# Kernel tuning notes

Hardware: AMD Instinct MI355X
Metric: run time of the kernel (lower is better)

## Reference

```python
import jax, jax.numpy as jnp
import numpy as np

L = 32      # num_layer
N_ORD = 64  # order_of_a_LTImodel
U = 64      # u_size
Y = 64      # y_size
T = 8192    # sequence length
SCALE = 0.05  # keep block-bidiagonal A spectrally stable over 8192 steps


def setup_inputs() -> dict:
    key = jax.random.key(0)
    k_u, k_a, k_b0, k_bl, k_c = jax.random.split(key, 5)
    inp = {
        "input": jax.random.normal(k_u, (T, U), dtype=jnp.float32),
        # per-layer A_i weights (diagonal blocks)
        "A_stack": jax.random.normal(k_a, (L, N_ORD, N_ORD), dtype=jnp.float32) * SCALE,
        # layer-0 B (maps u -> state)
        "B0": jax.random.normal(k_b0, (N_ORD, U), dtype=jnp.float32) * SCALE,
        # layer i>=1 B weights (sub-diagonal coupling blocks)
        "B_lower": jax.random.normal(k_bl, (L - 1, N_ORD, N_ORD), dtype=jnp.float32) * SCALE,
        # per-layer C_i weights, concatenated along columns in forward
        "C_stack": jax.random.normal(k_c, (L, Y, N_ORD), dtype=jnp.float32),
        # D is frozen zeros (feedthrough=False)
        "D_w": jnp.zeros((Y, U), dtype=jnp.float32),
    }
    return inp


def _assemble(A_stack, B0, B_lower, C_stack):
    l, n, _ = A_stack.shape
    S = l * n
    A = jnp.zeros((S, S), A_stack.dtype)
    for i in range(l):  # fixed small structural loop
        A = A.at[i * n:(i + 1) * n, i * n:(i + 1) * n].set(A_stack[i])
    for i in range(1, l):
        A = A.at[i * n:(i + 1) * n, (i - 1) * n:i * n].set(B_lower[i - 1])
    B = jnp.concatenate([B0, jnp.zeros((S - n, B0.shape[1]), B0.dtype)], axis=0)
    # torch.cat([C_i], dim=1): [Y, L*n]
    C = jnp.transpose(C_stack, (1, 0, 2)).reshape(C_stack.shape[1], S)
    return A, B, C


def reference(input, A_stack, B0, B_lower, C_stack, D_w):
    A, B, C = _assemble(A_stack, B0, B_lower, C_stack)
    S = A.shape[0]
    x0 = jnp.zeros((S,), input.dtype)

    def step(x, u):
        y = C @ x + D_w @ u      # output BEFORE state update (y_t uses x_t)
        x_next = A @ x + B @ u
        return x_next, y

    _, ys = jax.lax.scan(step, x0, input)
    return ys  # [T, Y]
```

## Files before the change

### kernel.cpp

```cpp
#include <hip/hip_runtime.h>


#define LYR 32
#define NO  64
#define TSEQ 8192
#define JT  16
#define KD  (JT*NO)
#define PROWS (TSEQ+JT)
#define PBUF ((size_t)PROWS*NO)
#define FD  4

typedef _Float16 h16;
typedef _Float16 h16x8 __attribute__((ext_vector_type(8)));
typedef float    f32x4 __attribute__((ext_vector_type(4)));

__global__ __launch_bounds__(256) void prep1(
    const float* __restrict__ u, const float* __restrict__ B0,
    const float* __restrict__ Bl, const float* __restrict__ Cst,
    h16* __restrict__ pall, h16* __restrict__ ccast, float* __restrict__ kf32)
{
    int idx = blockIdx.x*256 + threadIdx.x;
    const int n_pad0 = JT*NO;
    const int n_u    = TSEQ*NO;
    const int n_c    = LYR*NO*NO;
    const int n_k    = LYR*NO*NO;
    const int n_zp   = 32*JT*NO;
    int total = n_pad0 + n_u + n_c + n_k + n_zp;
    for (; idx < total; idx += gridDim.x*256) {
        int e = idx;
        if (e < n_pad0) { pall[e] = (h16)0.f; continue; }
        e -= n_pad0;
        if (e < n_u) { pall[n_pad0 + e] = (h16)u[e]; continue; }
        e -= n_u;
        if (e < n_c) { ccast[e] = (h16)Cst[e]; continue; }
        e -= n_c;
        if (e < n_k) {
            int i = e >> 12;
            int r = e & 4095;
            kf32[((size_t)i*JT)*4096 + r] = (i == 0) ? B0[r] : Bl[e - 4096];
            continue;
        }
        e -= n_k;
        int b = e >> 10;
        int off = e & 1023;
        pall[(size_t)(b+1)*PBUF + off] = (h16)0.f;
    }
}

__global__ __launch_bounds__(256) void build_step(
    const float* __restrict__ A_stack, float* __restrict__ kf32,
    float* __restrict__ apow, int s)
{
    int h = 1 << s;
    int extra = (s < 3) ? 1 : 0;
    int slots = h + extra;
    int layer = blockIdx.x / slots;
    int q     = blockIdx.x % slots;
    const float* X = (s == 0) ? (A_stack + (size_t)layer*4096)
                              : (apow + ((size_t)layer*4 + (s-1))*4096);
    const float* Yop;
    float* Z;
    if (q < h) { Yop = kf32 + ((size_t)layer*JT + q)*4096;
                 Z   = kf32 + ((size_t)layer*JT + h + q)*4096; }
    else       { Yop = X;
                 Z   = apow + ((size_t)layer*4 + s)*4096; }

    __shared__ float lx[64*68];
    __shared__ float ly[64*68];
    int tid = threadIdx.x;
    for (int e = tid; e < 4096; e += 256) {
        int r = e >> 6, c = e & 63;
        lx[r*68 + c] = X[e];
        ly[r*68 + c] = Yop[e];
    }
    __syncthreads();
    int r0 = (tid >> 4) << 2;
    int c0 = (tid & 15) << 2;
    float acc[4][4] = {};
    for (int k = 0; k < 64; k++) {
        float a0 = lx[(r0+0)*68 + k];
        float a1 = lx[(r0+1)*68 + k];
        float a2 = lx[(r0+2)*68 + k];
        float a3 = lx[(r0+3)*68 + k];
        f32x4 bv = *(const f32x4*)&ly[k*68 + c0];
        #pragma unroll
        for (int j = 0; j < 4; j++) {
            acc[0][j] += a0*bv[j]; acc[1][j] += a1*bv[j];
            acc[2][j] += a2*bv[j]; acc[3][j] += a3*bv[j];
        }
    }
    #pragma unroll
    for (int i2 = 0; i2 < 4; i2++) {
        f32x4 o; o[0]=acc[i2][0]; o[1]=acc[i2][1]; o[2]=acc[i2][2]; o[3]=acc[i2][3];
        *(f32x4*)&Z[(size_t)(r0+i2)*64 + c0] = o;
    }
}

__global__ __launch_bounds__(256) void castK(const float* __restrict__ kf32,
                                             h16* __restrict__ kt)
{
    int idx = blockIdx.x*256 + threadIdx.x;
    const int total = LYR*NO*KD;
    for (; idx < total; idx += gridDim.x*256) {
        int i   = idx >> 16;
        int rem = idx & 65535;
        int n   = rem >> 10;
        int kap = rem & 1023;
        int jp  = kap >> 6, m = kap & 63;
        int j   = JT-1-jp;
        kt[idx] = (h16)kf32[(((size_t)i*JT + j)*64 + n)*64 + m];
    }
}

template<int S>
__device__ __forceinline__ void phase_body(
    const h16* inb, h16* outb, const h16* __restrict__ kb,
    h16* __restrict__ gout, const int w0, float* red, const int tid)
{
    const int wv = tid >> 6, lane = tid & 63, r = lane & 15, q = lane >> 4;
    const h16* abase = inb + (r + wv*4)*72 + q*8;
    const h16* bbase = kb + (size_t)r*KD + wv*256 + q*8;
#define LDA(s, ls) (*(const h16x8*)(abase + ((s)*16 + ((ls)>>1))*72 + ((ls)&1)*32))
#define LDB(c, ls) (*(const h16x8*)(bbase + (c)*(16*KD) + (ls)*32))
    f32x4 acc[S][4] = {};
    h16x8 a0[S], b0[4], a1[S], b1[4];
    #pragma unroll
    for (int s = 0; s < S; s++) { a0[s]=LDA(s,0); a1[s]=LDA(s,1); }
    #pragma unroll
    for (int c = 0; c < 4; c++) { b0[c]=LDB(c,0); b1[c]=LDB(c,1); }
    #pragma unroll 1
    for (int h2 = 0; h2 < 4; h2++) {
        int pE = 2*h2 + 2; pE = pE > 7 ? 7 : pE;
        int pO = 2*h2 + 3; pO = pO > 7 ? 7 : pO;
        h16x8 ca[S], cb[4];
        #pragma unroll
        for (int s = 0; s < S; s++) ca[s] = a0[s];
        #pragma unroll
        for (int c = 0; c < 4; c++) cb[c] = b0[c];
        #pragma unroll
        for (int s = 0; s < S; s++) a0[s] = LDA(s, pE);
        #pragma unroll
        for (int c = 0; c < 4; c++) b0[c] = LDB(c, pE);
        #pragma unroll
        for (int s = 0; s < S; s++)
            #pragma unroll
            for (int c = 0; c < 4; c++)
                acc[s][c] = __builtin_amdgcn_mfma_f32_16x16x32_f16(ca[s], cb[c], acc[s][c], 0,0,0);
        #pragma unroll
        for (int s = 0; s < S; s++) ca[s] = a1[s];
        #pragma unroll
        for (int c = 0; c < 4; c++) cb[c] = b1[c];
        #pragma unroll
        for (int s = 0; s < S; s++) a1[s] = LDA(s, pO);
        #pragma unroll
        for (int c = 0; c < 4; c++) b1[c] = LDB(c, pO);
        #pragma unroll
        for (int s = 0; s < S; s++)
            #pragma unroll
            for (int c = 0; c < 4; c++)
                acc[s][c] = __builtin_amdgcn_mfma_f32_16x16x32_f16(ca[s], cb[c], acc[s][c], 0,0,0);
    }
#undef LDA
#undef LDB
    const int cb2 = (tid & 7) << 3;
    #pragma unroll
    for (int ch = 0; ch < (S+1)/2; ch++) {
        const int sbase = ch*2;
        const int nt = (S - sbase) < 2 ? (S - sbase) : 2;
        __syncthreads();
        if (wv >= 2) {
            float* myred = red + (size_t)(wv-2)*(32*68);
            #pragma unroll
            for (int s2 = 0; s2 < 2; s2++) if (s2 < nt)
                #pragma unroll
                for (int c = 0; c < 4; c++)
                    #pragma unroll
                    for (int g = 0; g < 4; g++)
                        myred[(s2*16 + q*4 + g)*68 + c*16 + r] = acc[sbase+s2][c][g];
        }
        __syncthreads();
        if (wv < 2) {
            float* myred = red + (size_t)wv*(32*68);
            #pragma unroll
            for (int s2 = 0; s2 < 2; s2++) if (s2 < nt)
                #pragma unroll
                for (int c = 0; c < 4; c++)
                    #pragma unroll
                    for (int g = 0; g < 4; g++)
                        myred[(s2*16 + q*4 + g)*68 + c*16 + r] += acc[sbase+s2][c][g];
        }
        __syncthreads();
        for (int w = tid >> 3; w < nt*16; w += 32) {
            f32x4 u0 = *(const f32x4*)&red[w*68 + cb2];
            f32x4 u1 = *(const f32x4*)&red[w*68 + cb2 + 4];
            f32x4 v0 = *(const f32x4*)&red[32*68 + w*68 + cb2];
            f32x4 v1 = *(const f32x4*)&red[32*68 + w*68 + cb2 + 4];
            u0 += v0; u1 += v1;
            h16 ov[8];
            #pragma unroll
            for (int j = 0; j < 4; j++) { ov[j] = (h16)u0[j]; ov[4+j] = (h16)u1[j]; }
            const int W = sbase*16 + w;
            if (outb) *(int4*)&outb[W*72 + cb2] = *(int4*)&ov[0];
            const unsigned wrel = (unsigned)(W - w0);
            if (wrel < 32u) *(int4*)&gout[(size_t)wrel*64 + cb2] = *(int4*)&ov[0];
        }
    }
    __syncthreads();
}

__global__ __launch_bounds__(256) void stage4(
    h16* pall, const h16* __restrict__ kt, int i0)
{
    __shared__ __align__(16) h16   bufA[96*72];
    __shared__ __align__(16) h16   bufB[96*72];
    __shared__ __align__(16) float red[2*32*68];
    const int tid = threadIdx.x;
    const size_t t0 = (size_t)blockIdx.x * 32;

    const h16* pin = pall + (size_t)i0*PBUF;
    for (int e = tid; e < 96*8; e += 256) {
        int rr = e >> 3, cc = e & 7;
        long g = (long)t0 - 48 + rr;
        int4 v = make_int4(0,0,0,0);
        if (g >= 0) v = *(const int4*)&pin[(size_t)g*64 + cc*8];
        *(int4*)&bufA[rr*72 + cc*8] = v;
    }
    __syncthreads();

    h16* g1 = pall + (size_t)(i0+1)*PBUF + (JT + t0)*64;
    h16* g2 = pall + (size_t)(i0+2)*PBUF + (JT + t0)*64;
    h16* g3 = pall + (size_t)(i0+3)*PBUF + (JT + t0)*64;
    h16* g4 = pall + (size_t)(i0+4)*PBUF + (JT + t0)*64;
    const h16* k1 = kt + (size_t)(i0+0)*NO*KD;
    const h16* k2 = kt + (size_t)(i0+1)*NO*KD;
    const h16* k3 = kt + (size_t)(i0+2)*NO*KD;
    const h16* k4 = kt + (size_t)(i0+3)*NO*KD;

    phase_body<5>(bufA, bufB, k1, g1, 48, red, tid);
    phase_body<4>(bufB, bufA, k2, g2, 32, red, tid);
    phase_body<3>(bufA, bufB, k3, g3, 16, red, tid);
    phase_body<2>(bufB, (h16*)0, k4, g4, 0, red, tid);
}

__global__ __launch_bounds__(256, 2) void y_final(
    const h16* __restrict__ pall, const h16* __restrict__ ccast,
    float* __restrict__ out)
{
    __shared__ __align__(16) float red[2*32*68];
    int tid = threadIdx.x;
    size_t t0 = (size_t)blockIdx.x * 32;
    int wv = tid >> 6, lane = tid & 63, r = lane & 15, q = lane >> 4;
    const h16* abase = pall + (size_t)(wv*8 + 1)*PBUF + (JT + t0 + r)*64 + q*8;
    const h16* bbase = ccast + (size_t)(wv*8)*4096 + (size_t)r*64 + q*8;
#define LDA2(s, ls) (*(const h16x8*)(abase + (size_t)((ls)>>1)*PBUF + (s)*(16*64) + ((ls)&1)*32))
#define LDB2(c, ls) (*(const h16x8*)(bbase + ((ls)>>1)*4096 + (c)*(16*64) + ((ls)&1)*32))
    f32x4 acc[2][4] = {};
    h16x8 a0[2], b0[4], a1[2], b1[4];
    #pragma unroll
    for (int s = 0; s < 2; s++) { a0[s]=LDA2(s,0); a1[s]=LDA2(s,1); }
    #pragma unroll
    for (int c = 0; c < 4; c++) { b0[c]=LDB2(c,0); b1[c]=LDB2(c,1); }
    #pragma unroll 1
    for (int h2 = 0; h2 < 8; h2++) {
        int pE = 2*h2 + 2; pE = pE > 15 ? 15 : pE;
        int pO = 2*h2 + 3; pO = pO > 15 ? 15 : pO;
        h16x8 ca[2], cb[4];
        #pragma unroll
        for (int s = 0; s < 2; s++) ca[s] = a0[s];
        #pragma unroll
        for (int c = 0; c < 4; c++) cb[c] = b0[c];
        #pragma unroll
        for (int s = 0; s < 2; s++) a0[s] = LDA2(s, pE);
        #pragma unroll
        for (int c = 0; c < 4; c++) b0[c] = LDB2(c, pE);
        #pragma unroll
        for (int s = 0; s < 2; s++)
            #pragma unroll
            for (int c = 0; c < 4; c++)
                acc[s][c] = __builtin_amdgcn_mfma_f32_16x16x32_f16(ca[s], cb[c], acc[s][c], 0,0,0);
        #pragma unroll
        for (int s = 0; s < 2; s++) ca[s] = a1[s];
        #pragma unroll
        for (int c = 0; c < 4; c++) cb[c] = b1[c];
        #pragma unroll
        for (int s = 0; s < 2; s++) a1[s] = LDA2(s, pO);
        #pragma unroll
        for (int c = 0; c < 4; c++) b1[c] = LDB2(c, pO);
        #pragma unroll
        for (int s = 0; s < 2; s++)
            #pragma unroll
            for (int c = 0; c < 4; c++)
                acc[s][c] = __builtin_amdgcn_mfma_f32_16x16x32_f16(ca[s], cb[c], acc[s][c], 0,0,0);
    }
#undef LDA2
#undef LDB2
    if (wv >= 2) {
        float* myred = red + (size_t)(wv-2)*(32*68);
        #pragma unroll
        for (int s = 0; s < 2; s++)
            #pragma unroll
            for (int c = 0; c < 4; c++)
                #pragma unroll
                for (int g = 0; g < 4; g++)
                    myred[(s*16 + q*4 + g)*68 + c*16 + r] = acc[s][c][g];
    }
    __syncthreads();
    if (wv < 2) {
        float* myred = red + (size_t)wv*(32*68);
        #pragma unroll
        for (int s = 0; s < 2; s++)
            #pragma unroll
            for (int c = 0; c < 4; c++)
                #pragma unroll
                for (int g = 0; g < 4; g++)
                    myred[(s*16 + q*4 + g)*68 + c*16 + r] += acc[s][c][g];
    }
    __syncthreads();
    int orow = tid >> 3, cb2 = (tid & 7) << 3;
    f32x4 u0 = *(const f32x4*)&red[orow*68 + cb2];
    f32x4 u1 = *(const f32x4*)&red[orow*68 + cb2 + 4];
    f32x4 v0 = *(const f32x4*)&red[32*68 + orow*68 + cb2];
    f32x4 v1 = *(const f32x4*)&red[32*68 + orow*68 + cb2 + 4];
    u0 += v0; u1 += v1;
    size_t obase = (t0 + orow)*64 + cb2;
    *(f32x4*)&out[obase]     = u0;
    *(f32x4*)&out[obase + 4] = u1;
}

extern "C" void kernel_launch(void* const* d_in, const int* in_sizes, int n_in,
                              void* d_out, int out_size, void* d_ws, size_t ws_size,
                              hipStream_t stream)
{
    const float* u   = (const float*)d_in[0];
    const float* Ast = (const float*)d_in[1];
    const float* B0  = (const float*)d_in[2];
    const float* Bl  = (const float*)d_in[3];
    const float* Cst = (const float*)d_in[4];
    float* out = (float*)d_out;
    (void)in_sizes; (void)n_in; (void)out_size; (void)ws_size;

    char* ws = (char*)d_ws;
    const size_t PBUF_BYTES = PBUF*sizeof(h16);
    h16*   pall  = (h16*)ws;
    h16*   ccast = (h16*)(ws + 33*PBUF_BYTES);
    h16*   kt    = (h16*)(ws + 33*PBUF_BYTES + 262144);
    float* kf32  = (float*)(ws + 33*PBUF_BYTES + 262144 + 4194304);
    float* apow  = (float*)(ws + 33*PBUF_BYTES + 262144 + 4194304 + 8388608);

    prep1<<<2048, 256, 0, stream>>>(u, B0, Bl, Cst, pall, ccast, kf32);
    for (int s = 0; s < 4; s++) {
        int h = 1 << s;
        int grid = 32*(h + (s < 3 ? 1 : 0));
        build_step<<<grid, 256, 0, stream>>>(Ast, kf32, apow, s);
    }
    castK<<<2048, 256, 0, stream>>>(kf32, kt);
    for (int i = 0; i < LYR; i += FD) {
        stage4<<<TSEQ/32, 256, 0, stream>>>(pall, kt, i);
    }
    y_final<<<TSEQ/32, 256, 0, stream>>>(pall, ccast, out);
}
```

Before: 325.8 us.

## Vectorize prep/cast kernels, deepen MFMA load prefetch, widen reduction chunks

The prep1 and castK kernels now move 8 or 4 elements per thread with 128-bit and 64-bit accesses instead of scalar ones, and prep1 launches fewer blocks. The MFMA inner loops in phase_body and y_final are fully unrolled with a deeper register prefetch: four B slices ahead in phase_body and four A and B slices ahead in y_final. The cross-wave reduction handles three sub-tiles per chunk instead of two, which enlarges the shared reduction buffer but needs fewer barrier rounds. The deeper prefetch raises register pressure, and the larger shared buffer may lower occupancy.

```diff
diff --git a/kernel.cpp b/kernel.cpp
--- a/kernel.cpp
+++ b/kernel.cpp
@@ -19,31 +19,51 @@
     const float* __restrict__ Bl, const float* __restrict__ Cst,
     h16* __restrict__ pall, h16* __restrict__ ccast, float* __restrict__ kf32)
 {
-    int idx = blockIdx.x*256 + threadIdx.x;
     const int n_pad0 = JT*NO;
     const int n_u    = TSEQ*NO;
     const int n_c    = LYR*NO*NO;
     const int n_k    = LYR*NO*NO;
     const int n_zp   = 32*JT*NO;
-    int total = n_pad0 + n_u + n_c + n_k + n_zp;
-    for (; idx < total; idx += gridDim.x*256) {
-        int e = idx;
-        if (e < n_pad0) { pall[e] = (h16)0.f; continue; }
+    const int total8 = (n_pad0 + n_u + n_c + n_k + n_zp) >> 3;
+    int idx8 = blockIdx.x*256 + threadIdx.x;
+    const int4 zero4 = make_int4(0,0,0,0);
+    for (; idx8 < total8; idx8 += gridDim.x*256) {
+        int e = idx8 << 3;
+        if (e < n_pad0) { *(int4*)&pall[e] = zero4; continue; }
         e -= n_pad0;
-        if (e < n_u) { pall[n_pad0 + e] = (h16)u[e]; continue; }
+        if (e < n_u) {
+            f32x4 f0 = *(const f32x4*)&u[e];
+            f32x4 f1 = *(const f32x4*)&u[e+4];
+            h16 ov[8];
+            #pragma unroll
+            for (int j = 0; j < 4; j++) { ov[j] = (h16)f0[j]; ov[4+j] = (h16)f1[j]; }
+            *(int4*)&pall[n_pad0 + e] = *(int4*)&ov[0];
+            continue;
+        }
         e -= n_u;
-        if (e < n_c) { ccast[e] = (h16)Cst[e]; continue; }
+        if (e < n_c) {
+            f32x4 f0 = *(const f32x4*)&Cst[e];
+            f32x4 f1 = *(const f32x4*)&Cst[e+4];
+            h16 ov[8];
+            #pragma unroll
+            for (int j = 0; j < 4; j++) { ov[j] = (h16)f0[j]; ov[4+j] = (h16)f1[j]; }
+            *(int4*)&ccast[e] = *(int4*)&ov[0];
+            continue;
+        }
         e -= n_c;
         if (e < n_k) {
             int i = e >> 12;
             int r = e & 4095;
-            kf32[((size_t)i*JT)*4096 + r] = (i == 0) ? B0[r] : Bl[e - 4096];
+            const float* src = (i == 0) ? &B0[r] : &Bl[e - 4096];
+            float* dst = &kf32[((size_t)i*JT)*4096 + r];
+            *(f32x4*)&dst[0] = *(const f32x4*)&src[0];
+            *(f32x4*)&dst[4] = *(const f32x4*)&src[4];
             continue;
         }
         e -= n_k;
         int b = e >> 10;
         int off = e & 1023;
-        pall[(size_t)(b+1)*PBUF + off] = (h16)0.f;
+        *(int4*)&pall[(size_t)(b+1)*PBUF + off] = zero4;
     }
 }
 
@@ -99,16 +119,21 @@
 __global__ __launch_bounds__(256) void castK(const float* __restrict__ kf32,
                                              h16* __restrict__ kt)
 {
-    int idx = blockIdx.x*256 + threadIdx.x;
-    const int total = LYR*NO*KD;
-    for (; idx < total; idx += gridDim.x*256) {
+    int idx4 = blockIdx.x*256 + threadIdx.x;
+    const int total4 = (LYR*NO*KD) >> 2;
+    for (; idx4 < total4; idx4 += gridDim.x*256) {
+        int idx = idx4 << 2;
         int i   = idx >> 16;
         int rem = idx & 65535;
         int n   = rem >> 10;
         int kap = rem & 1023;
         int jp  = kap >> 6, m = kap & 63;
         int j   = JT-1-jp;
-        kt[idx] = (h16)kf32[(((size_t)i*JT + j)*64 + n)*64 + m];
+        f32x4 f = *(const f32x4*)&kf32[(((size_t)i*JT + j)*64 + n)*64 + m];
+        h16 ov[4];
+        #pragma unroll
+        for (int t = 0; t < 4; t++) ov[t] = (h16)f[t];
+        *(int2*)&kt[idx] = *(int2*)&ov[0];
     }
 }
 
@@ -123,37 +148,30 @@
 #define LDA(s, ls) (*(const h16x8*)(abase + ((s)*16 + ((ls)>>1))*72 + ((ls)&1)*32))
 #define LDB(c, ls) (*(const h16x8*)(bbase + (c)*(16*KD) + (ls)*32))
     f32x4 acc[S][4] = {};
-    h16x8 a0[S], b0[4], a1[S], b1[4];
-    #pragma unroll
-    for (int s = 0; s < S; s++) { a0[s]=LDA(s,0); a1[s]=LDA(s,1); }
-    #pragma unroll
-    for (int c = 0; c < 4; c++) { b0[c]=LDB(c,0); b1[c]=LDB(c,1); }
-    #pragma unroll 1
-    for (int h2 = 0; h2 < 4; h2++) {
-        int pE = 2*h2 + 2; pE = pE > 7 ? 7 : pE;
-        int pO = 2*h2 + 3; pO = pO > 7 ? 7 : pO;
+    h16x8 a[2][S], b[4][4];
+    #pragma unroll
+    for (int ls = 0; ls < 2; ls++)
+        #pragma unroll
+        for (int s = 0; s < S; s++) a[ls][s] = LDA(s, ls);
+    #pragma unroll
+    for (int ls = 0; ls < 4; ls++)
+        #pragma unroll
+        for (int c = 0; c < 4; c++) b[ls][c] = LDB(c, ls);
+    #pragma unroll
+    for (int ls = 0; ls < 8; ls++) {
         h16x8 ca[S], cb[4];
         #pragma unroll
-        for (int s = 0; s < S; s++) ca[s] = a0[s];
-        #pragma unroll
-        for (int c = 0; c < 4; c++) cb[c] = b0[c];
-        #pragma unroll
-        for (int s = 0; s < S; s++) a0[s] = LDA(s, pE);
-        #pragma unroll
-        for (int c = 0; c < 4; c++) b0[c] = LDB(c, pE);
-        #pragma unroll
-        for (int s = 0; s < S; s++)
-            #pragma unroll
-            for (int c = 0; c < 4; c++)
-                acc[s][c] = __builtin_amdgcn_mfma_f32_16x16x32_f16(ca[s], cb[c], acc[s][c], 0,0,0);
-        #pragma unroll
-        for (int s = 0; s < S; s++) ca[s] = a1[s];
-        #pragma unroll
-        for (int c = 0; c < 4; c++) cb[c] = b1[c];
-        #pragma unroll
-        for (int s = 0; s < S; s++) a1[s] = LDA(s, pO);
-        #pragma unroll
-        for (int c = 0; c < 4; c++) b1[c] = LDB(c, pO);
+        for (int s = 0; s < S; s++) ca[s] = a[ls&1][s];
+        #pragma unroll
+        for (int c = 0; c < 4; c++) cb[c] = b[ls&3][c];
+        if (ls < 6) {
+            #pragma unroll
+            for (int s = 0; s < S; s++) a[ls&1][s] = LDA(s, ls+2);
+        }
+        if (ls < 4) {
+            #pragma unroll
+            for (int c = 0; c < 4; c++) b[ls&3][c] = LDB(c, ls+4);
+        }
         #pragma unroll
         for (int s = 0; s < S; s++)
             #pragma unroll
@@ -164,14 +182,14 @@
 #undef LDB
     const int cb2 = (tid & 7) << 3;
     #pragma unroll
-    for (int ch = 0; ch < (S+1)/2; ch++) {
-        const int sbase = ch*2;
-        const int nt = (S - sbase) < 2 ? (S - sbase) : 2;
+    for (int ch = 0; ch < (S+2)/3; ch++) {
+        const int sbase = ch*3;
+        const int nt = (S - sbase) < 3 ? (S - sbase) : 3;
         __syncthreads();
         if (wv >= 2) {
-            float* myred = red + (size_t)(wv-2)*(32*68);
-            #pragma unroll
-            for (int s2 = 0; s2 < 2; s2++) if (s2 < nt)
+            float* myred = red + (size_t)(wv-2)*(48*68);
+            #pragma unroll
+            for (int s2 = 0; s2 < 3; s2++) if (s2 < nt)
                 #pragma unroll
                 for (int c = 0; c < 4; c++)
                     #pragma unroll
@@ -180,9 +198,9 @@
         }
         __syncthreads();
         if (wv < 2) {
-            float* myred = red + (size_t)wv*(32*68);
-            #pragma unroll
-            for (int s2 = 0; s2 < 2; s2++) if (s2 < nt)
+            float* myred = red + (size_t)wv*(48*68);
+            #pragma unroll
+            for (int s2 = 0; s2 < 3; s2++) if (s2 < nt)
                 #pragma unroll
                 for (int c = 0; c < 4; c++)
                     #pragma unroll
@@ -193,8 +211,8 @@
         for (int w = tid >> 3; w < nt*16; w += 32) {
             f32x4 u0 = *(const f32x4*)&red[w*68 + cb2];
             f32x4 u1 = *(const f32x4*)&red[w*68 + cb2 + 4];
-            f32x4 v0 = *(const f32x4*)&red[32*68 + w*68 + cb2];
-            f32x4 v1 = *(const f32x4*)&red[32*68 + w*68 + cb2 + 4];
+            f32x4 v0 = *(const f32x4*)&red[48*68 + w*68 + cb2];
+            f32x4 v1 = *(const f32x4*)&red[48*68 + w*68 + cb2 + 4];
             u0 += v0; u1 += v1;
             h16 ov[8];
             #pragma unroll
@@ -213,7 +231,7 @@
 {
     __shared__ __align__(16) h16   bufA[96*72];
     __shared__ __align__(16) h16   bufB[96*72];
-    __shared__ __align__(16) float red[2*32*68];
+    __shared__ __align__(16) float red[2*48*68];
     const int tid = threadIdx.x;
     const size_t t0 = (size_t)blockIdx.x * 32;
 
@@ -255,37 +273,27 @@
 #define LDA2(s, ls) (*(const h16x8*)(abase + (size_t)((ls)>>1)*PBUF + (s)*(16*64) + ((ls)&1)*32))
 #define LDB2(c, ls) (*(const h16x8*)(bbase + ((ls)>>1)*4096 + (c)*(16*64) + ((ls)&1)*32))
     f32x4 acc[2][4] = {};
-    h16x8 a0[2], b0[4], a1[2], b1[4];
-    #pragma unroll
-    for (int s = 0; s < 2; s++) { a0[s]=LDA2(s,0); a1[s]=LDA2(s,1); }
-    #pragma unroll
-    for (int c = 0; c < 4; c++) { b0[c]=LDB2(c,0); b1[c]=LDB2(c,1); }
-    #pragma unroll 1
-    for (int h2 = 0; h2 < 8; h2++) {
-        int pE = 2*h2 + 2; pE = pE > 15 ? 15 : pE;
-        int pO = 2*h2 + 3; pO = pO > 15 ? 15 : pO;
+    h16x8 a[4][2], b[4][4];
+    #pragma unroll
+    for (int ls = 0; ls < 4; ls++) {
+        #pragma unroll
+        for (int s = 0; s < 2; s++) a[ls][s] = LDA2(s, ls);
+        #pragma unroll
+        for (int c = 0; c < 4; c++) b[ls][c] = LDB2(c, ls);
+    }
+    #pragma unroll
+    for (int ls = 0; ls < 16; ls++) {
         h16x8 ca[2], cb[4];
         #pragma unroll
-        for (int s = 0; s < 2; s++) ca[s] = a0[s];
-        #pragma unroll
-        for (int c = 0; c < 4; c++) cb[c] = b0[c];
-        #pragma unroll
-        for (int s = 0; s < 2; s++) a0[s] = LDA2(s, pE);
-        #pragma unroll
-        for (int c = 0; c < 4; c++) b0[c] = LDB2(c, pE);
-        #pragma unroll
-        for (int s = 0; s < 2; s++)
-            #pragma unroll
-            for (int c = 0; c < 4; c++)
-                acc[s][c] = __builtin_amdgcn_mfma_f32_16x16x32_f16(ca[s], cb[c], acc[s][c], 0,0,0);
-        #pragma unroll
-        for (int s = 0; s < 2; s++) ca[s] = a1[s];
-        #pragma unroll
-        for (int c = 0; c < 4; c++) cb[c] = b1[c];
-        #pragma unroll
-        for (int s = 0; s < 2; s++) a1[s] = LDA2(s, pO);
-        #pragma unroll
-        for (int c = 0; c < 4; c++) b1[c] = LDB2(c, pO);
+        for (int s = 0; s < 2; s++) ca[s] = a[ls&3][s];
+        #pragma unroll
+        for (int c = 0; c < 4; c++) cb[c] = b[ls&3][c];
+        if (ls < 12) {
+            #pragma unroll
+            for (int s = 0; s < 2; s++) a[ls&3][s] = LDA2(s, ls+4);
+            #pragma unroll
+            for (int c = 0; c < 4; c++) b[ls&3][c] = LDB2(c, ls+4);
+        }
         #pragma unroll
         for (int s = 0; s < 2; s++)
             #pragma unroll
@@ -347,7 +355,7 @@
     float* kf32  = (float*)(ws + 33*PBUF_BYTES + 262144 + 4194304);
     float* apow  = (float*)(ws + 33*PBUF_BYTES + 262144 + 4194304 + 8388608);
 
-    prep1<<<2048, 256, 0, stream>>>(u, B0, Bl, Cst, pall, ccast, kf32);
+    prep1<<<512, 256, 0, stream>>>(u, B0, Bl, Cst, pall, ccast, kf32);
     for (int s = 0; s < 4; s++) {
         int h = 1 << s;
         int grid = 32*(h + (s < 3 ? 1 : 0));
```

New measurement: 306.9 us. 5.8% less time.
